# Kernel optimization log

Measured on AMD Instinct MI355X. Metric: run time of the kernel, lower is better.

## Reference

```python
import jax, jax.numpy as jnp
import numpy as np

B, S, H, NH = 4, 1024, 1024, 16
DH = H // NH
EPS = 1e-12  # BERT layer_norm_eps


def layer_norm(x, scale, bias, eps=EPS):
    mu = jnp.mean(x, axis=-1, keepdims=True)
    var = jnp.var(x, axis=-1, keepdims=True)
    return (x - mu) / jnp.sqrt(var + eps) * scale + bias


def setup_inputs() -> dict:
    key = jax.random.key(0)
    ks = jax.random.split(key, 8)
    lin = lambda k: jax.random.normal(k, (H, H), jnp.float32) * 0.02
    zeros_h = jnp.zeros((H,), jnp.float32)
    return {
        "hidden_states": jax.random.normal(ks[0], (B, S, H), jnp.float32),
        "group_prob": jnp.zeros((B, S, S), jnp.float32),
        "attention_mask": jnp.ones((B, 1, S, S), jnp.int32),
        "Wq": lin(ks[1]), "bq": zeros_h,
        "Wk": lin(ks[2]), "bk": zeros_h,
        "Wv": lin(ks[3]), "bv": zeros_h,
        "gWq": lin(ks[4]), "gbq": zeros_h,
        "gWk": lin(ks[5]), "gbk": zeros_h,
        "g_ln_scale": jnp.ones((H,), jnp.float32), "g_ln_bias": zeros_h,
        "Wo": lin(ks[6]), "bo": zeros_h,
        "out_ln_scale": jnp.ones((H,), jnp.float32), "out_ln_bias": zeros_h,
    }


def _forward(hidden_states, group_prob, attention_mask, Wq, bq, Wk, bk, Wv, bv,
             gWq, gbq, gWk, gbk, g_ln_scale, g_ln_bias, Wo, bo,
             out_ln_scale, out_ln_bias):
    am = attention_mask.astype(jnp.int32)              # [B,1,S,S]
    a = jnp.eye(S, k=1, dtype=jnp.int32)               # superdiagonal
    b = jnp.eye(S, dtype=jnp.int32)                    # identity
    c = jnp.eye(S, k=-1, dtype=jnp.int32)              # subdiagonal
    tri = jnp.triu(jnp.ones((S, S), jnp.float32))      # upper tri incl diag

    # ---- GroupAttention (tree-transformer constituent priors) ----
    hs = layer_norm(hidden_states, g_ln_scale, g_ln_bias)
    gq = hs @ gWq.T + gbq
    gk = hs @ gWk.T + gbk
    g_scores = jnp.einsum('bqd,bkd->bqk', gq, gk) / jnp.float32(H)
    g_mask = (am & (a + c))[:, 0]                      # [B,S,S] tridiag band, no diag
    g_scores = jnp.where(g_mask == 0, -jnp.inf, g_scores)
    n_attn = jnp.nan_to_num(jax.nn.softmax(g_scores, axis=-1))
    n_attn = jnp.sqrt(n_attn * jnp.swapaxes(n_attn, -1, -2) + 1e-9)
    n_attn = group_prob + (1.0 - group_prob) * n_attn  # prior mixing
    t = jnp.where(a == 0, 0.0, jnp.log(n_attn + 1e-9)) @ tri
    g_attn = jnp.exp(tri @ t)
    strict_upper = tri.astype(jnp.int32) - b           # nonzero on strict upper tri
    g_attn = jnp.where(strict_upper == 0, 0.0, g_attn)
    g_attn = g_attn + jnp.swapaxes(g_attn, -1, -2) + jnp.where(b == 0, 1e-9, n_attn)
    break_prob = n_attn

    # ---- BertSelfAttention, mode 'L' ----
    def split_heads(x):
        return x.reshape(B, S, NH, DH).transpose(0, 2, 1, 3)  # [B,NH,S,DH]
    q = split_heads(hidden_states @ Wq.T + bq)
    k = split_heads(hidden_states @ Wk.T + bk)
    v = split_heads(hidden_states @ Wv.T + bv)
    scores = jnp.einsum('bhqd,bhkd->bhqk', q, k) / jnp.sqrt(jnp.float32(DH))
    keep = (am | b) != 0                               # diag always attended
    scores = jnp.where(keep, scores, -jnp.inf)
    probs = jax.nn.softmax(scores, axis=-1)
    probs = probs * g_attn[:, None]                    # group-prob reweighting
    ctx = jnp.einsum('bhqk,bhkd->bhqd', probs, v)
    ctx = ctx.transpose(0, 2, 1, 3).reshape(B, S, H)

    # ---- BertSelfOutput: dense + residual + LayerNorm ----
    out = layer_norm(ctx @ Wo.T + bo + hidden_states, out_ln_scale, out_ln_bias)
    return out, scores, g_attn, break_prob


def reference(hidden_states, group_prob, attention_mask, Wq, bq, Wk, bk, Wv, bv,
              gWq, gbq, gWk, gbk, g_ln_scale, g_ln_bias, Wo, bo,
              out_ln_scale, out_ln_bias):
    return _forward(hidden_states, group_prob, attention_mask, Wq, bq, Wk, bk,
                    Wv, bv, gWq, gbq, gWk, gbk, g_ln_scale, g_ln_bias, Wo, bo,
                    out_ln_scale, out_ln_bias)
```

## Files before the change

### kernel.cpp

```cpp
#include <hip/hip_runtime.h>
#include <math.h>

#define BB 4
#define S 1024
#define H 1024
#define NHD 16
#define DH 64
#define LN_EPS 1e-12f
#define SQ9 3.1622776601683795e-5f
#define NEG_INF (-__builtin_inff())
#define L2E 1.4426950408889634f

typedef unsigned short u16;
typedef unsigned int u32;
using bfrag = __attribute__((ext_vector_type(8))) short;
using f32x4 = __attribute__((ext_vector_type(4))) float;

typedef __attribute__((address_space(1))) void void_g;
typedef __attribute__((address_space(3))) void void_l;

__device__ __forceinline__ void gload16(const void* g, void* l) {
  __builtin_amdgcn_global_load_lds((void_g*)g, (void_l*)l, 16, 0, 0);
}

__device__ __forceinline__ u16 f2bf(float f) {
  u32 u = __builtin_bit_cast(u32, f);
  u32 r = (u + 0x7fffu + ((u >> 16) & 1u)) >> 16;
  return (u16)r;
}
__device__ __forceinline__ float bf2f(u32 b) {
  u32 u = b << 16;
  return __builtin_bit_cast(float, u);
}

__device__ __forceinline__ float block_sum256(float v, float* buf) {
#pragma unroll
  for (int o = 32; o > 0; o >>= 1) v += __shfl_down(v, o);
  if ((threadIdx.x & 63) == 0) buf[threadIdx.x >> 6] = v;
  __syncthreads();
  float r = buf[0] + buf[1] + buf[2] + buf[3];
  __syncthreads();
  return r;
}

__global__ __launch_bounds__(256) void prep_kernel(
    const float* __restrict__ Wq, const float* __restrict__ Wk, const float* __restrict__ Wv,
    const float* __restrict__ gWq, const float* __restrict__ gWk,
    const float* __restrict__ hidden, const int* __restrict__ am,
    const float* __restrict__ glns, const float* __restrict__ glnb,
    u16* __restrict__ dstW, u32* __restrict__ amb, u16* __restrict__ hsbf) {
  __shared__ float buf[4];
  int bid = blockIdx.x;
  if (bid < 9216) {
    const int WQ = 262144;
    int i = bid * 256 + threadIdx.x;
    const float* src; int off;
    if      (i < 1 * WQ) { src = Wq;  off = 0; }
    else if (i < 2 * WQ) { src = Wk;  off = 1 * WQ; }
    else if (i < 3 * WQ) { src = Wv;  off = 2 * WQ; }
    else if (i < 4 * WQ) { src = gWq; off = 3 * WQ; }
    else if (i < 5 * WQ) { src = gWk; off = 4 * WQ; }
    else                 { src = hidden; off = 5 * WQ; }
    float4 v = reinterpret_cast<const float4*>(src)[i - off];
    u32 lo = (u32)f2bf(v.x) | ((u32)f2bf(v.y) << 16);
    u32 hi = (u32)f2bf(v.z) | ((u32)f2bf(v.w) << 16);
    reinterpret_cast<uint2*>(dstW)[i] = make_uint2(lo, hi);
  } else if (bid < 25600) {
    size_t t = (size_t)(bid - 9216) * 256 + threadIdx.x;
    int v = am[t] != 0;
    unsigned long long m = __ballot(v);
    int lane = threadIdx.x & 63;
    if (lane == 0)       amb[t >> 5] = (u32)m;
    else if (lane == 32) amb[t >> 5] = (u32)(m >> 32);
  } else {
    size_t row = bid - 25600;
    const float4 xv = reinterpret_cast<const float4*>(hidden + row * H)[threadIdx.x];
    float s  = xv.x + xv.y + xv.z + xv.w;
    float s2 = xv.x * xv.x + xv.y * xv.y + xv.z * xv.z + xv.w * xv.w;
    s  = block_sum256(s, buf);
    s2 = block_sum256(s2, buf);
    float mu  = s * (1.0f / H);
    float var = s2 * (1.0f / H) - mu * mu;
    float inv = rsqrtf(var + LN_EPS);
    const float4 sv = reinterpret_cast<const float4*>(glns)[threadIdx.x];
    const float4 bv = reinterpret_cast<const float4*>(glnb)[threadIdx.x];
    float o0 = (xv.x - mu) * inv * sv.x + bv.x;
    float o1 = (xv.y - mu) * inv * sv.y + bv.y;
    float o2 = (xv.z - mu) * inv * sv.z + bv.z;
    float o3 = (xv.w - mu) * inv * sv.w + bv.w;
    u32 lo = (u32)f2bf(o0) | ((u32)f2bf(o1) << 16);
    u32 hi = (u32)f2bf(o2) | ((u32)f2bf(o3) << 16);
    reinterpret_cast<uint2*>(hsbf + row * H)[threadIdx.x] = make_uint2(lo, hi);
  }
}

__global__ __launch_bounds__(256) void mega_gemm(
    const u16* __restrict__ hbf, const u16* __restrict__ hsbf,
    const u16* __restrict__ Wcat,
    const float* __restrict__ bq, const float* __restrict__ bk, const float* __restrict__ bv,
    const float* __restrict__ gbq, const float* __restrict__ gbk,
    u16* __restrict__ q, u16* __restrict__ k, u16* __restrict__ vt,
    u16* __restrict__ gq, u16* __restrict__ gk) {
  __shared__ __align__(16) u16 SM[32768];
  const int Kdim = H;
  int fid = blockIdx.x + blockIdx.y * 40;
  int swz = (fid & 7) * 160 + (fid >> 3);
  int lx = swz % 40, ly = swz / 40;
  int which = lx >> 3;
  const u16* A = (which < 3) ? hbf : hsbf;
  int rowBlk = ly * 128, colBlk = lx * 128;
  int tid = threadIdx.x, wid = tid >> 6, l = tid & 63;
  int dr = l >> 3, sl = l & 7;
  int co = (sl ^ dr) << 3;
  const u16* Ag = A + (size_t)rowBlk * Kdim;
  const u16* Bg = Wcat + (size_t)colBlk * Kdim;
  f32x4 acc[4][4];
#pragma unroll
  for (int i = 0; i < 4; ++i)
#pragma unroll
    for (int j = 0; j < 4; ++j) acc[i][j] = (f32x4){0.f, 0.f, 0.f, 0.f};
#pragma unroll
  for (int i = 0; i < 4; ++i) {
    int L = wid * 4 + i;
    gload16(Ag + (size_t)(L * 8 + dr) * Kdim + co, &SM[L * 512]);
    gload16(Bg + (size_t)(L * 8 + dr) * Kdim + co, &SM[16384 + L * 512]);
  }
  __syncthreads();
  int wm = wid >> 1, wn = wid & 1;
  const int nt = Kdim >> 6;
  int buf = 0;
  int sw = (l & 7) << 4;
  for (int t = 0; t < nt; ++t) {
    if (t + 1 < nt) {
      int k0 = (t + 1) << 6;
      int dstoff = (buf ^ 1) * 8192;
#pragma unroll
      for (int i = 0; i < 4; ++i) {
        int L = wid * 4 + i;
        gload16(Ag + (size_t)(L * 8 + dr) * Kdim + k0 + co, &SM[dstoff + L * 512]);
        gload16(Bg + (size_t)(L * 8 + dr) * Kdim + k0 + co, &SM[16384 + dstoff + L * 512]);
      }
    }
    const char* Ab = (const char*)&SM[buf * 8192];
    const char* Bb = (const char*)&SM[16384 + buf * 8192];
#pragma unroll
    for (int ks = 0; ks < 2; ++ks) {
      int kb = (ks * 64 + ((l >> 4) << 4)) ^ sw;
      bfrag af[4], bfv[4];
#pragma unroll
      for (int mi = 0; mi < 4; ++mi)
        af[mi] = *(const bfrag*)(Ab + (wm * 64 + mi * 16 + (l & 15)) * 128 + kb);
#pragma unroll
      for (int ni = 0; ni < 4; ++ni)
        bfv[ni] = *(const bfrag*)(Bb + (wn * 64 + ni * 16 + (l & 15)) * 128 + kb);
#pragma unroll
      for (int mi = 0; mi < 4; ++mi)
#pragma unroll
        for (int ni = 0; ni < 4; ++ni)
          acc[mi][ni] = __builtin_amdgcn_mfma_f32_16x16x32_bf16(af[mi], bfv[ni], acc[mi][ni], 0, 0, 0);
    }
    __syncthreads();
    buf ^= 1;
  }
  const float* bias = (which == 0) ? bq : (which == 1) ? bk : (which == 2) ? bv
                      : (which == 3) ? gbq : gbk;
  if (which == 2) {
    u16* T = SM;
#pragma unroll
    for (int mi = 0; mi < 4; ++mi) {
#pragma unroll
      for (int ni = 0; ni < 4; ++ni) {
        int c = wn * 64 + ni * 16 + (l & 15);
        float bvv = bias[(colBlk & 1023) + c];
        int tokb = wm * 64 + mi * 16 + ((l >> 4) << 2);
        u32 w0 = (u32)f2bf(acc[mi][ni][0] + bvv) | ((u32)f2bf(acc[mi][ni][1] + bvv) << 16);
        u32 w1 = (u32)f2bf(acc[mi][ni][2] + bvv) | ((u32)f2bf(acc[mi][ni][3] + bvv) << 16);
        *(u32*)&T[c * 144 + tokb]     = w0;
        *(u32*)&T[c * 144 + tokb + 2] = w1;
      }
    }
    __syncthreads();
    int col = tid >> 1, th = tid & 1;
    int g = (colBlk & 1023) + col;
    int bb = rowBlk >> 10;
    int s0 = (rowBlk & 1023) + th * 64;
    const uint4* src = (const uint4*)&T[col * 144 + th * 64];
    u16* dst = vt + ((size_t)(bb * 1024 + g)) * S + s0;
#pragma unroll
    for (int i = 0; i < 8; ++i) reinterpret_cast<uint4*>(dst)[i] = src[i];
  } else {
    u16* O = (which == 0) ? q : (which == 1) ? k : (which == 3) ? gq : gk;
#pragma unroll
    for (int mi = 0; mi < 4; ++mi) {
#pragma unroll
      for (int ni = 0; ni < 4; ++ni) {
        int col = (colBlk + wn * 64 + ni * 16 + (l & 15)) & 1023;
        float bvv = bias[col];
#pragma unroll
        for (int j = 0; j < 4; ++j) {
          int row = rowBlk + wm * 64 + mi * 16 + ((l >> 4) << 2) + j;
          O[(size_t)row * H + col] = f2bf(acc[mi][ni][j] + bvv);
        }
      }
    }
  }
}

__global__ __launch_bounds__(256) void gemm_dense(
    const u16* __restrict__ A, const u16* __restrict__ Bw,
    const float* __restrict__ bias, const float* __restrict__ resid,
    u16* __restrict__ C) {
  __shared__ __align__(16) u16 SM[32768];
  const int Kdim = H;
  int fid = blockIdx.x + blockIdx.y * 8;
  int swz = (fid & 7) * 32 + (fid >> 3);
  int lx = swz & 7, ly = swz >> 3;
  int rowBlk = ly * 128, colBlk = lx * 128;
  int tid = threadIdx.x, wid = tid >> 6, l = tid & 63;
  int dr = l >> 3, sl = l & 7;
  int co = (sl ^ dr) << 3;
  const u16* Ag = A + (size_t)rowBlk * Kdim;
  const u16* Bg = Bw + (size_t)colBlk * Kdim;
  f32x4 acc[4][4];
#pragma unroll
  for (int i = 0; i < 4; ++i)
#pragma unroll
    for (int j = 0; j < 4; ++j) acc[i][j] = (f32x4){0.f, 0.f, 0.f, 0.f};
#pragma unroll
  for (int i = 0; i < 4; ++i) {
    int L = wid * 4 + i;
    gload16(Ag + (size_t)(L * 8 + dr) * Kdim + co, &SM[L * 512]);
    gload16(Bg + (size_t)(L * 8 + dr) * Kdim + co, &SM[16384 + L * 512]);
  }
  __syncthreads();
  int wm = wid >> 1, wn = wid & 1;
  const int nt = Kdim >> 6;
  int buf = 0;
  int sw = (l & 7) << 4;
  for (int t = 0; t < nt; ++t) {
    if (t + 1 < nt) {
      int k0 = (t + 1) << 6;
      int dstoff = (buf ^ 1) * 8192;
#pragma unroll
      for (int i = 0; i < 4; ++i) {
        int L = wid * 4 + i;
        gload16(Ag + (size_t)(L * 8 + dr) * Kdim + k0 + co, &SM[dstoff + L * 512]);
        gload16(Bg + (size_t)(L * 8 + dr) * Kdim + k0 + co, &SM[16384 + dstoff + L * 512]);
      }
    }
    const char* Ab = (const char*)&SM[buf * 8192];
    const char* Bb = (const char*)&SM[16384 + buf * 8192];
#pragma unroll
    for (int ks = 0; ks < 2; ++ks) {
      int kb = (ks * 64 + ((l >> 4) << 4)) ^ sw;
      bfrag af[4], bfv[4];
#pragma unroll
      for (int mi = 0; mi < 4; ++mi)
        af[mi] = *(const bfrag*)(Ab + (wm * 64 + mi * 16 + (l & 15)) * 128 + kb);
#pragma unroll
      for (int ni = 0; ni < 4; ++ni)
        bfv[ni] = *(const bfrag*)(Bb + (wn * 64 + ni * 16 + (l & 15)) * 128 + kb);
#pragma unroll
      for (int mi = 0; mi < 4; ++mi)
#pragma unroll
        for (int ni = 0; ni < 4; ++ni)
          acc[mi][ni] = __builtin_amdgcn_mfma_f32_16x16x32_bf16(af[mi], bfv[ni], acc[mi][ni], 0, 0, 0);
    }
    __syncthreads();
    buf ^= 1;
  }
#pragma unroll
  for (int mi = 0; mi < 4; ++mi) {
#pragma unroll
    for (int ni = 0; ni < 4; ++ni) {
      int col = colBlk + wn * 64 + ni * 16 + (l & 15);
      float bvv = bias[col];
#pragma unroll
      for (int j = 0; j < 4; ++j) {
        int row = rowBlk + wm * 64 + mi * 16 + ((l >> 4) << 2) + j;
        C[(size_t)row * H + col] = f2bf(acc[mi][ni][j] + bvv + resid[(size_t)row * H + col]);
      }
    }
  }
}

__global__ __launch_bounds__(256) void band_dots_kernel(
    const u16* __restrict__ gq, const u16* __restrict__ gk,
    const float* __restrict__ Wo, u16* __restrict__ Wobf,
    float* __restrict__ znext, float* __restrict__ zprev) {
  __shared__ float buf[4];
  int bid = blockIdx.x;
  if (bid >= 4096) {
    int i = (bid - 4096) * 256 + threadIdx.x;
    float4 v = reinterpret_cast<const float4*>(Wo)[i];
    u32 lo = (u32)f2bf(v.x) | ((u32)f2bf(v.y) << 16);
    u32 hi = (u32)f2bf(v.z) | ((u32)f2bf(v.w) << 16);
    reinterpret_cast<uint2*>(Wobf)[i] = make_uint2(lo, hi);
    return;
  }
  size_t idx = bid;
  int i = (int)(idx & (S - 1));
  uint2 q2 = reinterpret_cast<const uint2*>(gq + idx * H)[threadIdx.x];
  float q0 = bf2f(q2.x & 0xffff), q1 = bf2f(q2.x >> 16);
  float q2f = bf2f(q2.y & 0xffff), q3 = bf2f(q2.y >> 16);
  float dn = 0.f, dp = 0.f;
  if (i < S - 1) {
    uint2 k2 = reinterpret_cast<const uint2*>(gk + (idx + 1) * H)[threadIdx.x];
    dn = q0 * bf2f(k2.x & 0xffff) + q1 * bf2f(k2.x >> 16) +
         q2f * bf2f(k2.y & 0xffff) + q3 * bf2f(k2.y >> 16);
  }
  if (i > 0) {
    uint2 k2 = reinterpret_cast<const uint2*>(gk + (idx - 1) * H)[threadIdx.x];
    dp = q0 * bf2f(k2.x & 0xffff) + q1 * bf2f(k2.x >> 16) +
         q2f * bf2f(k2.y & 0xffff) + q3 * bf2f(k2.y >> 16);
  }
  dn = block_sum256(dn, buf);
  dp = block_sum256(dp, buf);
  if (threadIdx.x == 0) { znext[idx] = dn; zprev[idx] = dp; }
}

__global__ __launch_bounds__(1024) void band_prefix_kernel(
    const float* __restrict__ znext, const float* __restrict__ zprev,
    const int* __restrict__ am, const float* __restrict__ gp,
    float* __restrict__ sband, float* __restrict__ Cpre) {
  __shared__ float pd[S];
  __shared__ float scn[S];
  int b = blockIdx.x, i = threadIdx.x;
  size_t idx = (size_t)b * S + i;
  bool luv = (i < S - 1) && (am[((size_t)b * S + i) * S + i + 1] != 0);
  bool ldv = (i > 0) && (am[((size_t)b * S + i) * S + i - 1] != 0);
  float pf, pdn;
  if (!luv && !ldv) { pf = 0.f; pdn = 0.f; }
  else if (!ldv)    { pf = 1.f; pdn = 0.f; }
  else if (!luv)    { pf = 0.f; pdn = 1.f; }
  else {
    float lu = znext[idx] * (1.0f / (float)H);
    float ld = zprev[idx] * (1.0f / (float)H);
    float m = fmaxf(lu, ld);
    float eu = expf(lu - m), ed = expf(ld - m);
    float inv = 1.f / (eu + ed);
    pf = eu * inv; pdn = ed * inv;
  }
  pd[i] = pdn;
  __syncthreads();
  float sb = 0.f, L = 0.f;
  if (i < S - 1) {
    sb = sqrtf(pf * pd[i + 1] + 1e-9f);
    float gpv = gp[((size_t)b * S + i) * S + (i + 1)];
    float nm = gpv + (1.f - gpv) * sb;
    L = logf(nm + 1e-9f);
  }
  sband[idx] = sb;
  scn[i] = L;
  __syncthreads();
  for (int off = 1; off < S; off <<= 1) {
    float t = (i >= off) ? scn[i - off] : 0.f;
    __syncthreads();
    scn[i] += t;
    __syncthreads();
  }
  Cpre[idx] = (i > 0) ? scn[i - 1] : 0.f;
}

__global__ __launch_bounds__(256) void gattn_write_kernel(
    const float* __restrict__ gp, const float* __restrict__ sband,
    const float* __restrict__ Cpre, float* __restrict__ ga, float* __restrict__ brk) {
  __shared__ float Crow[S];
  __shared__ float Srow[S];
  size_t bi = blockIdx.x;
  int b = (int)(bi >> 10), i = (int)(bi & (S - 1));
  reinterpret_cast<float4*>(Crow)[threadIdx.x] =
      reinterpret_cast<const float4*>(Cpre + (size_t)b * S)[threadIdx.x];
  reinterpret_cast<float4*>(Srow)[threadIdx.x] =
      reinterpret_cast<const float4*>(sband + (size_t)b * S)[threadIdx.x];
  __syncthreads();
  float Ci = Crow[i];
  size_t rowoff = bi * S;
  const float4 g4 = reinterpret_cast<const float4*>(gp + rowoff)[threadIdx.x];
  const float gparr[4] = {g4.x, g4.y, g4.z, g4.w};
  float go[4], bo_[4];
#pragma unroll
  for (int j = 0; j < 4; ++j) {
    int k = threadIdx.x * 4 + j;
    float gpv = gparr[j];
    float gav;
    if (k == i) {
      gav = gpv + (1.f - gpv) * SQ9;
    } else {
      float d = (k > i) ? (Crow[k] - Ci) : (Ci - Crow[k]);
      gav = expf(d) + 1e-9f;
    }
    float sval = (k == i + 1) ? Srow[i] : ((k == i - 1) ? Srow[k] : SQ9);
    go[j]  = gav;
    bo_[j] = gpv + (1.f - gpv) * sval;
  }
  f32x4 go4 = (f32x4){go[0], go[1], go[2], go[3]};
  __builtin_nontemporal_store(go4, reinterpret_cast<f32x4*>(ga + rowoff) + threadIdx.x);
  f32x4 bo4 = (f32x4){bo_[0], bo_[1], bo_[2], bo_[3]};
  __builtin_nontemporal_store(bo4, reinterpret_cast<f32x4*>(brk + rowoff) + threadIdx.x);
}

__global__ __launch_bounds__(512) void flash_kernel(
    const u16* __restrict__ q, const u16* __restrict__ k, const u16* __restrict__ vt,
    const u32* __restrict__ amb, const float* __restrict__ Cpre,
    const float* __restrict__ gp,
    float* __restrict__ scores, u16* __restrict__ ctx) {
  __shared__ __align__(16) u16 QPt[8192];
  __shared__ __align__(16) u16 Kt[2][4096];
  __shared__ __align__(16) u16 Vt[2][4096];
  __shared__ float CLds[1024];
  int fid = blockIdx.x + blockIdx.y * 8;
  int qb = (fid >> 3) & 7;
  int bh = (fid & 7) * 8 + (fid >> 6);
  int b = bh >> 4, h = bh & 15;
  int tid = threadIdx.x, wid = tid >> 6, l = tid & 63;
  int dr = l >> 3, sl = l & 7;
  int co = (sl ^ dr) << 3;
  const u16* qbase = q + ((size_t)b * S + qb * 128) * H + h * 64;
  const u16* kbase = k + (size_t)b * S * H + h * 64;
  const u16* vtb   = vt + (size_t)bh * 64 * S;
  {
    float2 c2 = reinterpret_cast<const float2*>(Cpre + (size_t)b * S)[tid];
    c2.x *= L2E; c2.y *= L2E;
    reinterpret_cast<float2*>(CLds)[tid] = c2;
  }
#pragma unroll
  for (int i = 0; i < 2; ++i) {
    int L = wid * 2 + i;
    gload16(qbase + (size_t)(L * 8 + dr) * H + co, &QPt[L * 512]);
  }
  gload16(kbase + (size_t)(wid * 8 + dr) * H + co, &Kt[0][wid * 512]);
  gload16(vtb + (size_t)(wid * 8 + dr) * S + co, &Vt[0][wid * 512]);
  __syncthreads();
  int sw = (l & 7) << 4;
  int qr = l & 15;
  bfrag qa[2];
#pragma unroll
  for (int ks = 0; ks < 2; ++ks) {
    int kb = (ks * 64 + ((l >> 4) << 4)) ^ sw;
    qa[ks] = *(const bfrag*)((const char*)QPt + (wid * 16 + qr) * 128 + kb);
  }
  __syncthreads();
  int rowg0 = qb * 128 + wid * 16 + ((l >> 4) << 2);
  float Ci2[4], gdiag[4];
#pragma unroll
  for (int j = 0; j < 4; ++j) {
    int row = rowg0 + j;
    Ci2[j] = CLds[row];
    float gpd = gp[((size_t)b * S + row) * S + row];
    gdiag[j] = gpd + (1.f - gpd) * SQ9;
  }
  float m_run[4], l_loc[4];
  f32x4 oacc[4];
#pragma unroll
  for (int j = 0; j < 4; ++j) { m_run[j] = NEG_INF; l_loc[j] = 0.f; }
#pragma unroll
  for (int nb = 0; nb < 4; ++nb) oacc[nb] = (f32x4){0.f, 0.f, 0.f, 0.f};
  int cur = 0;
  for (int kt = 0; kt < 16; ++kt) {
    if (kt < 15) {
      gload16(kbase + (size_t)((kt + 1) * 64 + wid * 8 + dr) * H + co, &Kt[cur ^ 1][wid * 512]);
      gload16(vtb + (size_t)(wid * 8 + dr) * S + (kt + 1) * 64 + co, &Vt[cur ^ 1][wid * 512]);
    }
    f32x4 acc[4];
#pragma unroll
    for (int nb = 0; nb < 4; ++nb) acc[nb] = (f32x4){0.f, 0.f, 0.f, 0.f};
    __builtin_amdgcn_s_setprio(1);
#pragma unroll
    for (int ks = 0; ks < 2; ++ks) {
      int kb = (ks * 64 + ((l >> 4) << 4)) ^ sw;
#pragma unroll
      for (int nb = 0; nb < 4; ++nb) {
        bfrag bv = *(const bfrag*)((const char*)Kt[cur] + (nb * 16 + qr) * 128 + kb);
        acc[nb] = __builtin_amdgcn_mfma_f32_16x16x32_bf16(qa[ks], bv, acc[nb], 0, 0, 0);
      }
    }
    __builtin_amdgcn_s_setprio(0);
    float vals[4][4];
    float tm[4] = {NEG_INF, NEG_INF, NEG_INF, NEG_INF};
#pragma unroll
    for (int j = 0; j < 4; ++j) {
      int row = rowg0 + j;
      uint2 w01 = *reinterpret_cast<const uint2*>(amb + ((size_t)b * S + row) * 32 + kt * 2);
      float* srow = scores + ((size_t)bh * S + row) * S + kt * 64;
#pragma unroll
      for (int nb = 0; nb < 4; ++nb) {
        int col = nb * 16 + qr;
        int colg = kt * 64 + col;
        u32 word = (nb < 2) ? w01.x : w01.y;
        int keep = (int)((word >> (col & 31)) & 1u) | (row == colg);
        float v = keep ? acc[nb][j] * 0.125f : NEG_INF;
        vals[nb][j] = v;
        __builtin_nontemporal_store(v, srow + col);
        tm[j] = fmaxf(tm[j], v);
      }
    }
#pragma unroll
    for (int j = 0; j < 4; ++j) {
#pragma unroll
      for (int o = 1; o < 16; o <<= 1) tm[j] = fmaxf(tm[j], __shfl_xor(tm[j], o));
    }
    float Ck2[4];
#pragma unroll
    for (int nb = 0; nb < 4; ++nb) Ck2[nb] = CLds[kt * 64 + nb * 16 + qr];
#pragma unroll
    for (int j = 0; j < 4; ++j) {
      int row = rowg0 + j;
      int prow = wid * 16 + ((l >> 4) << 2) + j;
      char* ptrow = (char*)QPt + prow * 128;
      int psw = (prow & 7) << 4;
      if (tm[j] > m_run[j] + 8.0f) {
        float sc = exp2f((m_run[j] - tm[j]) * L2E);
        m_run[j] = tm[j];
        l_loc[j] *= sc;
#pragma unroll
        for (int nb = 0; nb < 4; ++nb) oacc[nb][j] *= sc;
      }
      float mn = m_run[j];
      float pp[4], pg[4];
      if (mn > NEG_INF) {
        float m2 = mn * L2E;
#pragma unroll
        for (int nb = 0; nb < 4; ++nb) {
          float t = __builtin_fmaf(vals[nb][j], L2E, -m2);
          pp[nb] = exp2f(t);
          int colg = kt * 64 + nb * 16 + qr;
          float d2 = (colg > row) ? (Ck2[nb] - Ci2[j]) : (Ci2[j] - Ck2[nb]);
          float g = exp2f(t + d2);
          pg[nb] = (colg == row) ? pp[nb] * gdiag[j] : g;
        }
      } else {
#pragma unroll
        for (int nb = 0; nb < 4; ++nb) { pp[nb] = 0.f; pg[nb] = 0.f; }
      }
      l_loc[j] += pp[0] + pp[1] + pp[2] + pp[3];
#pragma unroll
      for (int nb = 0; nb < 4; ++nb)
        *(u16*)(ptrow + (((nb * 16 + qr) * 2) ^ psw)) = f2bf(pg[nb]);
    }
    __builtin_amdgcn_s_setprio(1);
#pragma unroll
    for (int ks = 0; ks < 2; ++ks) {
      int kb = (ks * 64 + ((l >> 4) << 4)) ^ sw;
      bfrag pa = *(const bfrag*)((const char*)QPt + (wid * 16 + qr) * 128 + kb);
#pragma unroll
      for (int nb = 0; nb < 4; ++nb) {
        bfrag vv = *(const bfrag*)((const char*)Vt[cur] + (nb * 16 + qr) * 128 + kb);
        oacc[nb] = __builtin_amdgcn_mfma_f32_16x16x32_bf16(pa, vv, oacc[nb], 0, 0, 0);
      }
    }
    __builtin_amdgcn_s_setprio(0);
    asm volatile("s_waitcnt vmcnt(16)" ::: "memory");
    __builtin_amdgcn_s_barrier();
    __builtin_amdgcn_sched_barrier(0);
    cur ^= 1;
  }
#pragma unroll
  for (int j = 0; j < 4; ++j) {
#pragma unroll
    for (int o = 1; o < 16; o <<= 1) l_loc[j] += __shfl_xor(l_loc[j], o);
  }
#pragma unroll
  for (int j = 0; j < 4; ++j) {
    int row = rowg0 + j;
    float ir = 1.f / l_loc[j];
#pragma unroll
    for (int nb = 0; nb < 4; ++nb) {
      int d = nb * 16 + qr;
      ctx[((size_t)b * S + row) * H + h * 64 + d] = f2bf(oacc[nb][j] * ir);
    }
  }
}

__global__ __launch_bounds__(256) void ln_bf_kernel(
    const u16* __restrict__ x, const float* __restrict__ sc,
    const float* __restrict__ bi, float* __restrict__ y) {
  __shared__ float buf[4];
  size_t row = blockIdx.x;
  uint2 xv = reinterpret_cast<const uint2*>(x + row * H)[threadIdx.x];
  float x0 = bf2f(xv.x & 0xffff), x1 = bf2f(xv.x >> 16);
  float x2 = bf2f(xv.y & 0xffff), x3 = bf2f(xv.y >> 16);
  float s  = x0 + x1 + x2 + x3;
  float s2 = x0 * x0 + x1 * x1 + x2 * x2 + x3 * x3;
  s  = block_sum256(s, buf);
  s2 = block_sum256(s2, buf);
  float mu  = s * (1.0f / H);
  float var = s2 * (1.0f / H) - mu * mu;
  float inv = rsqrtf(var + LN_EPS);
  const float4 sv = reinterpret_cast<const float4*>(sc)[threadIdx.x];
  const float4 bv = reinterpret_cast<const float4*>(bi)[threadIdx.x];
  float4 o;
  o.x = (x0 - mu) * inv * sv.x + bv.x;
  o.y = (x1 - mu) * inv * sv.y + bv.y;
  o.z = (x2 - mu) * inv * sv.z + bv.z;
  o.w = (x3 - mu) * inv * sv.w + bv.w;
  reinterpret_cast<float4*>(y + row * H)[threadIdx.x] = o;
}

extern "C" void kernel_launch(void* const* d_in, const int* in_sizes, int n_in,
                              void* d_out, int out_size, void* d_ws, size_t ws_size,
                              hipStream_t stream) {
  const float* hidden = (const float*)d_in[0];
  const float* gp     = (const float*)d_in[1];
  const int*   am     = (const int*)d_in[2];
  const float* Wq = (const float*)d_in[3];  const float* bq = (const float*)d_in[4];
  const float* Wk = (const float*)d_in[5];  const float* bk = (const float*)d_in[6];
  const float* Wv = (const float*)d_in[7];  const float* bv = (const float*)d_in[8];
  const float* gWq = (const float*)d_in[9]; const float* gbq = (const float*)d_in[10];
  const float* gWk = (const float*)d_in[11];const float* gbk = (const float*)d_in[12];
  const float* glns = (const float*)d_in[13]; const float* glnb = (const float*)d_in[14];
  const float* Wo = (const float*)d_in[15]; const float* bo = (const float*)d_in[16];
  const float* olns = (const float*)d_in[17]; const float* olnb = (const float*)d_in[18];

  float* out    = (float*)d_out;
  float* scores = out + (size_t)BB * S * H;
  float* gattn  = scores + (size_t)BB * NHD * S * S;
  float* brk    = gattn + (size_t)BB * S * S;

  const size_t MB = 1u << 20;
  char* w = (char*)d_ws;
  u16* Wcat  = (u16*)(w);
  u16* hbf   = (u16*)(w + 10 * MB);
  u16* ctxbf = hbf;
  u16* hsbf  = (u16*)(w + 18 * MB);
  u16* Wobf  = hsbf;
  u16* qbf   = (u16*)(w + 26 * MB);
  u16* kbf   = (u16*)(w + 34 * MB);
  u16* vtb   = (u16*)(w + 42 * MB);
  u16* gqbf  = (u16*)(w + 50 * MB);
  u16* densebf = gqbf;
  u16* gkbf  = (u16*)(w + 58 * MB);
  u32* amb   = (u32*)(w + 66 * MB);
  float* znext  = (float*)(w + 66 * MB + 512 * 1024);
  float* zprev  = znext + BB * S;
  float* sbandA = zprev + BB * S;
  float* CpreA  = sbandA + BB * S;

  dim3 blk(256);

  prep_kernel<<<29696, blk, 0, stream>>>(Wq, Wk, Wv, gWq, gWk, hidden, am,
                                         glns, glnb, Wcat, amb, hsbf);

  mega_gemm<<<dim3(40, 32), blk, 0, stream>>>(hbf, hsbf, Wcat,
                                              bq, bk, bv, gbq, gbk,
                                              qbf, kbf, vtb, gqbf, gkbf);

  band_dots_kernel<<<5120, blk, 0, stream>>>(gqbf, gkbf, Wo, Wobf, znext, zprev);
  band_prefix_kernel<<<BB, 1024, 0, stream>>>(znext, zprev, am, gp, sbandA, CpreA);
  gattn_write_kernel<<<BB * S, blk, 0, stream>>>(gp, sbandA, CpreA, gattn, brk);

  flash_kernel<<<dim3(8, 64), dim3(512), 0, stream>>>(qbf, kbf, vtb, amb, CpreA,
                                                      gp, scores, ctxbf);

  gemm_dense<<<dim3(8, 32), blk, 0, stream>>>(ctxbf, Wobf, bo, hidden, densebf);
  ln_bf_kernel<<<BB * S, blk, 0, stream>>>(densebf, olns, olnb, out);
}
```

Measured before the change: 246.3 us.

## Fuse group-attention write kernel into flash kernel as extra workgroups

Merges the gattn/break_prob writer into the flash attention launch by appending 2048 extra 512-thread workgroups, each handling two rows of the group-attention outputs. The intent is to drop one kernel launch and let the memory-bound writes overlap with the compute-bound flash workgroups on otherwise idle CUs. The cost is that the writer blocks now reserve the flash kernel's full shared-memory footprint and register budget, which may cut their occupancy. The flash block index is also flattened to 1D.

```diff
diff --git a/kernel.cpp b/kernel.cpp
--- a/kernel.cpp
+++ b/kernel.cpp
@@ -10,6 +10,7 @@
 #define SQ9 3.1622776601683795e-5f
 #define NEG_INF (-__builtin_inff())
 #define L2E 1.4426950408889634f
+#define FLASH_NWG 512
 
 typedef unsigned short u16;
 typedef unsigned int u32;
@@ -362,58 +363,65 @@
   Cpre[idx] = (i > 0) ? scn[i - 1] : 0.f;
 }
 
-__global__ __launch_bounds__(256) void gattn_write_kernel(
-    const float* __restrict__ gp, const float* __restrict__ sband,
-    const float* __restrict__ Cpre, float* __restrict__ ga, float* __restrict__ brk) {
-  __shared__ float Crow[S];
-  __shared__ float Srow[S];
-  size_t bi = blockIdx.x;
-  int b = (int)(bi >> 10), i = (int)(bi & (S - 1));
-  reinterpret_cast<float4*>(Crow)[threadIdx.x] =
-      reinterpret_cast<const float4*>(Cpre + (size_t)b * S)[threadIdx.x];
-  reinterpret_cast<float4*>(Srow)[threadIdx.x] =
-      reinterpret_cast<const float4*>(sband + (size_t)b * S)[threadIdx.x];
-  __syncthreads();
-  float Ci = Crow[i];
-  size_t rowoff = bi * S;
-  const float4 g4 = reinterpret_cast<const float4*>(gp + rowoff)[threadIdx.x];
-  const float gparr[4] = {g4.x, g4.y, g4.z, g4.w};
-  float go[4], bo_[4];
-#pragma unroll
-  for (int j = 0; j < 4; ++j) {
-    int k = threadIdx.x * 4 + j;
-    float gpv = gparr[j];
-    float gav;
-    if (k == i) {
-      gav = gpv + (1.f - gpv) * SQ9;
-    } else {
-      float d = (k > i) ? (Crow[k] - Ci) : (Ci - Crow[k]);
-      gav = expf(d) + 1e-9f;
-    }
-    float sval = (k == i + 1) ? Srow[i] : ((k == i - 1) ? Srow[k] : SQ9);
-    go[j]  = gav;
-    bo_[j] = gpv + (1.f - gpv) * sval;
-  }
-  f32x4 go4 = (f32x4){go[0], go[1], go[2], go[3]};
-  __builtin_nontemporal_store(go4, reinterpret_cast<f32x4*>(ga + rowoff) + threadIdx.x);
-  f32x4 bo4 = (f32x4){bo_[0], bo_[1], bo_[2], bo_[3]};
-  __builtin_nontemporal_store(bo4, reinterpret_cast<f32x4*>(brk + rowoff) + threadIdx.x);
-}
-
-__global__ __launch_bounds__(512) void flash_kernel(
+__global__ __launch_bounds__(512) void flash_gattn_kernel(
     const u16* __restrict__ q, const u16* __restrict__ k, const u16* __restrict__ vt,
     const u32* __restrict__ amb, const float* __restrict__ Cpre,
-    const float* __restrict__ gp,
-    float* __restrict__ scores, u16* __restrict__ ctx) {
+    const float* __restrict__ sband, const float* __restrict__ gp,
+    float* __restrict__ scores, u16* __restrict__ ctx,
+    float* __restrict__ ga, float* __restrict__ brk) {
   __shared__ __align__(16) u16 QPt[8192];
   __shared__ __align__(16) u16 Kt[2][4096];
   __shared__ __align__(16) u16 Vt[2][4096];
   __shared__ float CLds[1024];
-  int fid = blockIdx.x + blockIdx.y * 8;
+  int tid = threadIdx.x;
+  if (blockIdx.x >= FLASH_NWG) {
+    int gbid = blockIdx.x - FLASH_NWG;
+    int r0 = gbid * 2;
+    int b = r0 >> 10;
+    float* Crow = (float*)QPt;
+    float* Srow = Crow + 1024;
+    reinterpret_cast<float2*>(Crow)[tid] =
+        reinterpret_cast<const float2*>(Cpre + (size_t)b * S)[tid];
+    reinterpret_cast<float2*>(Srow)[tid] =
+        reinterpret_cast<const float2*>(sband + (size_t)b * S)[tid];
+    __syncthreads();
+    int half = tid >> 8;
+    int row = r0 + half;
+    int i = row & (S - 1);
+    float Ci = Crow[i];
+    float Scur = Srow[i];
+    float Sprev = (i > 0) ? Srow[i - 1] : 0.f;
+    size_t rowoff = (size_t)row * S;
+    int c0 = (tid & 255) * 4;
+    float4 g4 = *reinterpret_cast<const float4*>(gp + rowoff + c0);
+    const float gparr[4] = {g4.x, g4.y, g4.z, g4.w};
+    float go[4], bo_[4];
+#pragma unroll
+    for (int j = 0; j < 4; ++j) {
+      int kk = c0 + j;
+      float gpv = gparr[j];
+      float gav;
+      if (kk == i) {
+        gav = gpv + (1.f - gpv) * SQ9;
+      } else {
+        float d = (kk > i) ? (Crow[kk] - Ci) : (Ci - Crow[kk]);
+        gav = expf(d) + 1e-9f;
+      }
+      float sval = (kk == i + 1) ? Scur : ((kk == i - 1) ? Sprev : SQ9);
+      go[j]  = gav;
+      bo_[j] = gpv + (1.f - gpv) * sval;
+    }
+    f32x4 go4 = (f32x4){go[0], go[1], go[2], go[3]};
+    __builtin_nontemporal_store(go4, reinterpret_cast<f32x4*>(ga + rowoff + c0));
+    f32x4 bo4 = (f32x4){bo_[0], bo_[1], bo_[2], bo_[3]};
+    __builtin_nontemporal_store(bo4, reinterpret_cast<f32x4*>(brk + rowoff + c0));
+    return;
+  }
+  int fid = blockIdx.x;
   int qb = (fid >> 3) & 7;
   int bh = (fid & 7) * 8 + (fid >> 6);
   int b = bh >> 4, h = bh & 15;
-  int tid = threadIdx.x, wid = tid >> 6, l = tid & 63;
+  int wid = tid >> 6, l = tid & 63;
   int dr = l >> 3, sl = l & 7;
   int co = (sl ^ dr) << 3;
   const u16* qbase = q + ((size_t)b * S + qb * 128) * H + h * 64;
@@ -647,10 +655,9 @@
 
   band_dots_kernel<<<5120, blk, 0, stream>>>(gqbf, gkbf, Wo, Wobf, znext, zprev);
   band_prefix_kernel<<<BB, 1024, 0, stream>>>(znext, zprev, am, gp, sbandA, CpreA);
-  gattn_write_kernel<<<BB * S, blk, 0, stream>>>(gp, sbandA, CpreA, gattn, brk);
-
-  flash_kernel<<<dim3(8, 64), dim3(512), 0, stream>>>(qbf, kbf, vtb, amb, CpreA,
-                                                      gp, scores, ctxbf);
+
+  flash_gattn_kernel<<<dim3(FLASH_NWG + 2048), dim3(512), 0, stream>>>(
+      qbf, kbf, vtb, amb, CpreA, sbandA, gp, scores, ctxbf, gattn, brk);
 
   gemm_dense<<<dim3(8, 32), blk, 0, stream>>>(ctxbf, Wobf, bo, hidden, densebf);
   ln_bf_kernel<<<BB * S, blk, 0, stream>>>(densebf, olns, olnb, out);
```

Result: no change. 248.4 us (+0.9%).
